# Kernel optimization log

Hardware: AMD Instinct MI355X
Metric: run time of the kernel (lower is better)

The kernel has to match this reference:

```python
import jax, jax.numpy as jnp
import numpy as np

IN_FEA = 128
OUT_FEA = 128
ALPHA = 0.2  # LeakyReLU negative slope
NEG_INF = -1.0e12


def setup_inputs() -> dict:
    key = jax.random.key(0)
    k1, k2, k3, k4 = jax.random.split(key, 4)
    b, n = 8, 2048
    inp = jax.random.normal(k1, (b, n, IN_FEA), dtype=jnp.float32)
    adj = jax.random.randint(k2, (b, n, n), 0, 2, dtype=jnp.int32)
    # xavier_uniform with gain=1.414
    def xavier(k, shape, gain=1.414):
        fan_in, fan_out = shape[0], shape[1]
        limit = gain * np.sqrt(6.0 / (fan_in + fan_out))
        return jax.random.uniform(k, shape, jnp.float32, -limit, limit)
    W = xavier(k3, (IN_FEA, OUT_FEA))
    a = xavier(k4, (2 * OUT_FEA, 1))
    return {"inp": inp, "adj": adj, "W": W, "a": a}


def reference(inp, adj, W, a):
    # h: [b, n, d]
    h = jnp.matmul(inp, W)
    # Original builds [b, n*n, 2d] via repeat/view; equivalently split a into
    # a1 (applied to h_j, the 'chunks' half) and a2 (applied to h_i).
    d = h.shape[-1]
    a1 = a[:d, 0]   # [d]
    a2 = a[d:, 0]   # [d]
    f1 = jnp.einsum('bnd,d->bn', h, a1)  # contributes per-column (j)
    f2 = jnp.einsum('bnd,d->bn', h, a2)  # contributes per-row (i)
    e = jax.nn.leaky_relu(f2[:, :, None] + f1[:, None, :], negative_slope=ALPHA)  # [b, n, n]
    logits = jnp.where(adj > 0, e, NEG_INF)
    attention = jax.nn.softmax(logits, axis=-1)
    out_h = jnp.matmul(attention, h)
    out_h = jax.nn.elu(out_h) + h  # concat=True branch
    return out_h
```

## Files before the change

### kernel.cpp

```cpp
#include <hip/hip_runtime.h>
#include <hip/hip_bf16.h>

typedef __bf16 bf16x8 __attribute__((ext_vector_type(8)));
typedef __bf16 bf16x4 __attribute__((ext_vector_type(4)));
typedef float  f32x4  __attribute__((ext_vector_type(4)));

#define LRELU_ALPHA 0.2f
#define LOG2E 1.44269504088896340736f

__device__ __forceinline__ float fexp2(float x) { return exp2f(x); }

__device__ __forceinline__ void wg_barrier() {
    asm volatile("s_waitcnt lgkmcnt(0)" ::: "memory");
    __builtin_amdgcn_s_barrier();
    asm volatile("" ::: "memory");
}

__global__ __launch_bounds__(128) void gat_prep(
    const float* __restrict__ inp, const float* __restrict__ W,
    const float* __restrict__ a,
    float* __restrict__ h, float* __restrict__ f1, float* __restrict__ f2)
{
    const int r0 = blockIdx.x << 3;
    const int d  = threadIdx.x;
    __shared__ float sIn[8][128];
    __shared__ float sRed[8][4];
    #pragma unroll
    for (int r = 0; r < 8; ++r)
        sIn[r][d] = inp[(size_t)(r0 + r) * 128 + d];
    __syncthreads();

    float acc[8] = {0.f,0.f,0.f,0.f,0.f,0.f,0.f,0.f};
    #pragma unroll 4
    for (int k = 0; k < 128; ++k) {
        float wv = W[k * 128 + d];
        #pragma unroll
        for (int r = 0; r < 8; ++r) acc[r] += sIn[r][k] * wv;
    }

    const float a1 = a[d], a2 = a[128 + d];
    const int wv = d >> 6;
    #pragma unroll
    for (int r = 0; r < 8; ++r) {
        h[(size_t)(r0 + r) * 128 + d] = acc[r];
        float t1 = acc[r] * a1;
        float t2 = acc[r] * a2;
        #pragma unroll
        for (int m = 1; m < 64; m <<= 1) {
            t1 += __shfl_xor(t1, m);
            t2 += __shfl_xor(t2, m);
        }
        if ((d & 63) == 0) { sRed[r][wv] = t1; sRed[r][2 + wv] = t2; }
    }
    __syncthreads();
    if (d < 8) {
        f1[r0 + d] = (sRed[d][0] + sRed[d][1]) * LOG2E;
        f2[r0 + d] = (sRed[d][2] + sRed[d][3]) * LOG2E;
    }
}

__global__ __launch_bounds__(256) void gat_f1max(
    const float* __restrict__ f1, float* __restrict__ f1max)
{
    const int b = blockIdx.x;
    const int t = threadIdx.x;
    float m = -1e30f;
    for (int j = t; j < 2048; j += 256) m = fmaxf(m, f1[b * 2048 + j]);
    #pragma unroll
    for (int k = 1; k < 64; k <<= 1) m = fmaxf(m, __shfl_xor(m, k));
    __shared__ float sm[4];
    if ((t & 63) == 0) sm[t >> 6] = m;
    __syncthreads();
    if (t == 0) f1max[b] = fmaxf(fmaxf(sm[0], sm[1]), fmaxf(sm[2], sm[3]));
}

__global__ __launch_bounds__(256) void gat_pack(
    const float* __restrict__ h, __bf16* __restrict__ pack)
{
    __shared__ __bf16 tile[64][74];
    const int tid = threadIdx.x;
    const int bidx = blockIdx.x;
    const int b  = bidx >> 6;
    const int tI = bidx & 63;
    const int n0 = (tI >> 1) << 6;
    const int d0 = (tI & 1) << 6;
    #pragma unroll
    for (int pass = 0; pass < 2; ++pass) {
        int row = (tid >> 3) + (pass << 5);
        int c   = (tid & 7) << 3;
        const float* src = h + (size_t)(b * 2048 + n0 + row) * 128 + d0 + c;
        float4 v0 = *(const float4*)src;
        float4 v1 = *(const float4*)(src + 4);
        __bf16* tp = &tile[row][c];
        tp[0]=(__bf16)v0.x; tp[1]=(__bf16)v0.y; tp[2]=(__bf16)v0.z; tp[3]=(__bf16)v0.w;
        tp[4]=(__bf16)v1.x; tp[5]=(__bf16)v1.y; tp[6]=(__bf16)v1.z; tp[7]=(__bf16)v1.w;
    }
    __syncthreads();
    const int lane = tid & 63;
    const int il = lane & 15;
    const int kg = lane >> 4;
    #pragma unroll
    for (int pass = 0; pass < 2; ++pass) {
        const int f  = (tid >> 6) + (pass << 2);
        const int Dl = f >> 1;
        const int jh = f & 1;
        union { __bf16 e[8]; bf16x8 v; } u;
        #pragma unroll
        for (int e = 0; e < 8; ++e)
            u.e[e] = tile[(jh << 5) + (kg << 3) + e][(Dl << 4) + il];
        const size_t off = (((size_t)(b << 5) + (n0 >> 6)) << 13)
                         + ((size_t)((((d0 >> 4) + Dl) << 1) | jh) << 9)
                         + (lane << 3);
        *(bf16x8*)(pack + off) = u.v;
    }
}

#define PCOMPUTE(TT, BUF) do {                                                \
    float4 fv = *(const float4*)&f1s[((TT) << 6) + (pj4 << 2)];               \
    float p0, p1, p2, p3;                                                     \
    { float x = f2v + fv.x; float e = fmaxf(x, LRELU_ALPHA * x) - Mshift;     \
      p0 = fexp2(__builtin_fmaf(e, (float)gA.x, -1000.f)); }                  \
    { float x = f2v + fv.y; float e = fmaxf(x, LRELU_ALPHA * x) - Mshift;     \
      p1 = fexp2(__builtin_fmaf(e, (float)gA.y, -1000.f)); }                  \
    { float x = f2v + fv.z; float e = fmaxf(x, LRELU_ALPHA * x) - Mshift;     \
      p2 = fexp2(__builtin_fmaf(e, (float)gA.z, -1000.f)); }                  \
    { float x = f2v + fv.w; float e = fmaxf(x, LRELU_ALPHA * x) - Mshift;     \
      p3 = fexp2(__builtin_fmaf(e, (float)gA.w, -1000.f)); }                  \
    bf16x4 pb;                                                                \
    pb[0] = (__bf16)p0; pb[1] = (__bf16)p1;                                   \
    pb[2] = (__bf16)p2; pb[3] = (__bf16)p3;                                   \
    den += (float)pb[0] + (float)pb[1] + (float)pb[2] + (float)pb[3];         \
    *(bf16x4*)(&Ps[BUF][pwo]) = pb;                                           \
} while (0)

__global__ __launch_bounds__(512, 4) void gat_attn5(
    const int* __restrict__ adj, const float* __restrict__ h,
    const __bf16* __restrict__ pack, const float* __restrict__ f1g,
    const float* __restrict__ f2g, const float* __restrict__ f1maxg,
    float* __restrict__ out)
{
    const int bid = ((blockIdx.x & 7) << 6) | (blockIdx.x >> 3);
    const int b  = bid >> 6;
    const int i0 = (bid & 63) << 5;
    const int tid = threadIdx.x;

    __shared__ float f1s[2048];
    __shared__ alignas(16) __bf16 Ps[2][2048];
    __shared__ float lsum[32];

    *(float4*)&f1s[tid << 2] = *(const float4*)&f1g[(b << 11) + (tid << 2)];

    const int pi  = tid >> 4;
    const int pj4 = tid & 15;
    const float fm  = f1maxg[b];
    const float f2v = f2g[(b << 11) + i0 + pi];
    const float Mshift = fmaxf(f2v + fm, LRELU_ALPHA * (f2v + fm)) - 1000.0f;
    const int* ajp = adj + (((size_t)(b << 11) + i0 + pi) << 11) + (pj4 << 2);
    const int pwo = (pi << 6) + ((((pj4 << 3)) ^ ((pi & 7) << 4)) >> 1);

    const int w    = tid >> 6;
    const int lane = tid & 63;
    const int il   = lane & 15;
    const int kg   = lane >> 4;
    const int ig   = w & 1;
    const int dq   = w >> 1;
    const int ai   = (ig << 4) + il;
    const int aof0 = (ai << 6) + (((kg << 4) ^ ((ai & 7) << 4)) >> 1);
    const int aof1 = (ai << 6) + (((64 | (kg << 4)) ^ ((ai & 7) << 4)) >> 1);
    const __bf16* pB = pack + (((size_t)b << 5) << 13) + (dq << 11) + (lane << 3);

    f32x4 acc0 = {0.f,0.f,0.f,0.f}, acc1 = {0.f,0.f,0.f,0.f};
    float den = 0.f;

    int4 gA  = *(const int4*)ajp;
    int4 gA2 = *(const int4*)(ajp + 64);
    bf16x8 Bc0 = *(const bf16x8*)(pB);
    bf16x8 Bc1 = *(const bf16x8*)(pB + 512);
    bf16x8 Bc2 = *(const bf16x8*)(pB + 1024);
    bf16x8 Bc3 = *(const bf16x8*)(pB + 1536);

    wg_barrier();

    PCOMPUTE(0, 0);
    gA = gA2;
    gA2 = *(const int4*)(ajp + 128);

    wg_barrier();

    for (int t = 0; t < 31; ++t) {
        const __bf16* pBn = pB + ((size_t)(t + 1) << 13);
        bf16x8 Bn0 = *(const bf16x8*)(pBn);
        bf16x8 Bn1 = *(const bf16x8*)(pBn + 512);
        bf16x8 Bn2 = *(const bf16x8*)(pBn + 1024);
        bf16x8 Bn3 = *(const bf16x8*)(pBn + 1536);

        bf16x8 A0 = *(const bf16x8*)(&Ps[t & 1][aof0]);
        bf16x8 A1 = *(const bf16x8*)(&Ps[t & 1][aof1]);

        PCOMPUTE(t + 1, (t + 1) & 1);
        gA = gA2;
        gA2 = *(const int4*)(ajp + (((t + 3) & 31) << 6));

        acc0 = __builtin_amdgcn_mfma_f32_16x16x32_bf16(A0, Bc0, acc0, 0, 0, 0);
        acc0 = __builtin_amdgcn_mfma_f32_16x16x32_bf16(A1, Bc1, acc0, 0, 0, 0);
        acc1 = __builtin_amdgcn_mfma_f32_16x16x32_bf16(A0, Bc2, acc1, 0, 0, 0);
        acc1 = __builtin_amdgcn_mfma_f32_16x16x32_bf16(A1, Bc3, acc1, 0, 0, 0);

        Bc0 = Bn0; Bc1 = Bn1; Bc2 = Bn2; Bc3 = Bn3;

        wg_barrier();
    }

    {
        bf16x8 A0 = *(const bf16x8*)(&Ps[1][aof0]);
        bf16x8 A1 = *(const bf16x8*)(&Ps[1][aof1]);
        acc0 = __builtin_amdgcn_mfma_f32_16x16x32_bf16(A0, Bc0, acc0, 0, 0, 0);
        acc0 = __builtin_amdgcn_mfma_f32_16x16x32_bf16(A1, Bc1, acc0, 0, 0, 0);
        acc1 = __builtin_amdgcn_mfma_f32_16x16x32_bf16(A0, Bc2, acc1, 0, 0, 0);
        acc1 = __builtin_amdgcn_mfma_f32_16x16x32_bf16(A1, Bc3, acc1, 0, 0, 0);
    }

    den += __shfl_xor(den, 1);
    den += __shfl_xor(den, 2);
    den += __shfl_xor(den, 4);
    den += __shfl_xor(den, 8);
    if (pj4 == 0) lsum[pi] = den;
    wg_barrier();

    #pragma unroll
    for (int r = 0; r < 4; ++r) {
        const int   row = (kg << 2) + r;
        const float dn  = lsum[(ig << 4) + row];
        const size_t gbase = (((size_t)(b << 11) + i0 + (ig << 4) + row) << 7)
                             + (dq << 5) + il;
        float v, e;
        v = acc0[r] / dn; e = (v > 0.f) ? v : (__expf(v) - 1.f); out[gbase]      = e + h[gbase];
        v = acc1[r] / dn; e = (v > 0.f) ? v : (__expf(v) - 1.f); out[gbase + 16] = e + h[gbase + 16];
    }
}

extern "C" void kernel_launch(void* const* d_in, const int* in_sizes, int n_in,
                              void* d_out, int out_size, void* d_ws, size_t ws_size,
                              hipStream_t stream)
{
    const float* inp = (const float*)d_in[0];
    const int*   adj = (const int*)d_in[1];
    const float* W   = (const float*)d_in[2];
    const float* a   = (const float*)d_in[3];
    float* out = (float*)d_out;

    char* ws = (char*)d_ws;
    float*  h     = (float*)ws;
    __bf16* pack  = (__bf16*)(ws + 8388608);
    float*  f1    = (float*)(ws + 8388608 + 4194304);
    float*  f2    = (float*)(ws + 8388608 + 4194304 + 65536);
    float*  f1max = (float*)(ws + 8388608 + 4194304 + 131072);

    gat_prep<<<2048, 128, 0, stream>>>(inp, W, a, h, f1, f2);
    gat_f1max<<<8, 256, 0, stream>>>(f1, f1max);
    gat_pack<<<512, 256, 0, stream>>>(h, pack);
    gat_attn5<<<512, 512, 0, stream>>>(adj, h, pack, f1, f2, f1max, out);
}
```

Baseline: 59.60 us.

## Bit-pack adjacency in a pre-pass and store h as bf16

Adds a gat_adjpack kernel that streams the int32 adjacency once and writes a 1-bit-per-edge mask in the nibble layout the attention kernel consumes. The attention kernel then reads one uint4 per thread instead of prefetching int4 adjacency tiles every iteration. h is now written once as bf16, which shrinks the pack and residual reads, and each wave now covers 32 rows by 16 features so B fragments load half as often. The full adjacency read still happens, just in a separate simple kernel, and the residual add now uses bf16-rounded h, which loses some precision.

```diff
diff --git a/kernel.cpp b/kernel.cpp
--- a/kernel.cpp
+++ b/kernel.cpp
@@ -19,7 +19,7 @@
 __global__ __launch_bounds__(128) void gat_prep(
     const float* __restrict__ inp, const float* __restrict__ W,
     const float* __restrict__ a,
-    float* __restrict__ h, float* __restrict__ f1, float* __restrict__ f2)
+    __bf16* __restrict__ hb, float* __restrict__ f1, float* __restrict__ f2)
 {
     const int r0 = blockIdx.x << 3;
     const int d  = threadIdx.x;
@@ -42,7 +42,7 @@
     const int wv = d >> 6;
     #pragma unroll
     for (int r = 0; r < 8; ++r) {
-        h[(size_t)(r0 + r) * 128 + d] = acc[r];
+        hb[(size_t)(r0 + r) * 128 + d] = (__bf16)acc[r];
         float t1 = acc[r] * a1;
         float t2 = acc[r] * a2;
         #pragma unroll
@@ -75,9 +75,9 @@
 }
 
 __global__ __launch_bounds__(256) void gat_pack(
-    const float* __restrict__ h, __bf16* __restrict__ pack)
-{
-    __shared__ __bf16 tile[64][74];
+    const __bf16* __restrict__ hb, __bf16* __restrict__ pack)
+{
+    __shared__ __bf16 tile[64][72];
     const int tid = threadIdx.x;
     const int bidx = blockIdx.x;
     const int b  = bidx >> 6;
@@ -88,12 +88,8 @@
     for (int pass = 0; pass < 2; ++pass) {
         int row = (tid >> 3) + (pass << 5);
         int c   = (tid & 7) << 3;
-        const float* src = h + (size_t)(b * 2048 + n0 + row) * 128 + d0 + c;
-        float4 v0 = *(const float4*)src;
-        float4 v1 = *(const float4*)(src + 4);
-        __bf16* tp = &tile[row][c];
-        tp[0]=(__bf16)v0.x; tp[1]=(__bf16)v0.y; tp[2]=(__bf16)v0.z; tp[3]=(__bf16)v0.w;
-        tp[4]=(__bf16)v1.x; tp[5]=(__bf16)v1.y; tp[6]=(__bf16)v1.z; tp[7]=(__bf16)v1.w;
+        *(bf16x8*)&tile[row][c] =
+            *(const bf16x8*)(hb + (size_t)(b * 2048 + n0 + row) * 128 + d0 + c);
     }
     __syncthreads();
     const int lane = tid & 63;
@@ -115,17 +111,78 @@
     }
 }
 
+__global__ __launch_bounds__(256) void gat_adjpack(
+    const int* __restrict__ adj, unsigned int* __restrict__ tb)
+{
+    __shared__ unsigned long long blt[16][8][4];
+    const int tid  = threadIdx.x;
+    const int w    = tid >> 6;
+    const int lane = tid & 63;
+    const int base = blockIdx.x << 4;
+
+    #pragma unroll
+    for (int rr = 0; rr < 4; ++rr) {
+        const int rloc = (w << 2) + rr;
+        const int* ap = adj + ((size_t)(base + rloc) << 11) + (lane << 2);
+        unsigned long long kept = 0ull;
+        #pragma unroll
+        for (int s = 0; s < 8; ++s) {
+            int4 v = *(const int4*)(ap + (s << 8));
+            unsigned long long b0 = __ballot(v.x > 0);
+            unsigned long long b1 = __ballot(v.y > 0);
+            unsigned long long b2 = __ballot(v.z > 0);
+            unsigned long long b3 = __ballot(v.w > 0);
+            const int e4 = lane & 3;
+            unsigned long long be = (e4 == 0) ? b0 : (e4 == 1) ? b1
+                                  : (e4 == 2) ? b2 : b3;
+            kept = ((lane >> 2) == s) ? be : kept;
+        }
+        if (lane < 32) blt[rloc][lane >> 2][lane & 3] = kept;
+    }
+    __syncthreads();
+
+    const int r   = tid >> 4;
+    const int pj4 = tid & 15;
+    unsigned int w0 = 0, w1 = 0, w2 = 0, w3 = 0;
+    #pragma unroll
+    for (int s = 0; s < 8; ++s) {
+        unsigned long long q0 = blt[r][s][0];
+        unsigned long long q1 = blt[r][s][1];
+        unsigned long long q2 = blt[r][s][2];
+        unsigned long long q3 = blt[r][s][3];
+        #pragma unroll
+        for (int tt = 0; tt < 4; ++tt) {
+            const int t = (s << 2) + tt;
+            const int L = (tt << 4) + pj4;
+            unsigned int nib = (unsigned int)((q0 >> L) & 1)
+                             | ((unsigned int)((q1 >> L) & 1) << 1)
+                             | ((unsigned int)((q2 >> L) & 1) << 2)
+                             | ((unsigned int)((q3 >> L) & 1) << 3);
+            const unsigned int sh = (unsigned int)((t & 7) << 2);
+            if (t < 8)       w0 |= nib << sh;
+            else if (t < 16) w1 |= nib << sh;
+            else if (t < 24) w2 |= nib << sh;
+            else             w3 |= nib << sh;
+        }
+    }
+    uint4 o; o.x = w0; o.y = w1; o.z = w2; o.w = w3;
+    *(uint4*)(tb + (((size_t)(base + r) << 4) + pj4) * 4) = o;
+}
+
 #define PCOMPUTE(TT, BUF) do {                                                \
     float4 fv = *(const float4*)&f1s[((TT) << 6) + (pj4 << 2)];               \
+    const unsigned int wv = ((TT) & 16) ? (((TT) & 8) ? aw.w : aw.z)          \
+                                        : (((TT) & 8) ? aw.y : aw.x);         \
+    const unsigned int nib = wv >> (((TT) & 7) << 2);                         \
     float p0, p1, p2, p3;                                                     \
-    { float x = f2v + fv.x; float e = fmaxf(x, LRELU_ALPHA * x) - Mshift;     \
-      p0 = fexp2(__builtin_fmaf(e, (float)gA.x, -1000.f)); }                  \
-    { float x = f2v + fv.y; float e = fmaxf(x, LRELU_ALPHA * x) - Mshift;     \
-      p1 = fexp2(__builtin_fmaf(e, (float)gA.y, -1000.f)); }                  \
-    { float x = f2v + fv.z; float e = fmaxf(x, LRELU_ALPHA * x) - Mshift;     \
-      p2 = fexp2(__builtin_fmaf(e, (float)gA.z, -1000.f)); }                  \
-    { float x = f2v + fv.w; float e = fmaxf(x, LRELU_ALPHA * x) - Mshift;     \
-      p3 = fexp2(__builtin_fmaf(e, (float)gA.w, -1000.f)); }                  \
+    { float x = f2v + fv.x; float e1 = fmaxf(x, LRELU_ALPHA * x) - Mshift;    \
+      p0 = fexp2(__builtin_fmaf(e1, (float)(nib & 1), -1000.f)); }            \
+    { float x = f2v + fv.y; float e1 = fmaxf(x, LRELU_ALPHA * x) - Mshift;    \
+      p1 = fexp2(__builtin_fmaf(e1, (float)((nib >> 1) & 1), -1000.f)); }     \
+    { float x = f2v + fv.z; float e1 = fmaxf(x, LRELU_ALPHA * x) - Mshift;    \
+      p2 = fexp2(__builtin_fmaf(e1, (float)((nib >> 2) & 1), -1000.f)); }     \
+    { float x = f2v + fv.w; float e1 = fmaxf(x, LRELU_ALPHA * x) - Mshift;    \
+      p3 = fexp2(__builtin_fmaf(e1, (float)((nib >> 3) & 1), -1000.f)); }     \
     bf16x4 pb;                                                                \
     pb[0] = (__bf16)p0; pb[1] = (__bf16)p1;                                   \
     pb[2] = (__bf16)p2; pb[3] = (__bf16)p3;                                   \
@@ -133,8 +190,8 @@
     *(bf16x4*)(&Ps[BUF][pwo]) = pb;                                           \
 } while (0)
 
-__global__ __launch_bounds__(512, 4) void gat_attn5(
-    const int* __restrict__ adj, const float* __restrict__ h,
+__global__ __launch_bounds__(512, 4) void gat_attn6(
+    const unsigned int* __restrict__ tb, const __bf16* __restrict__ hb,
     const __bf16* __restrict__ pack, const float* __restrict__ f1g,
     const float* __restrict__ f2g, const float* __restrict__ f1maxg,
     float* __restrict__ out)
@@ -155,35 +212,27 @@
     const float fm  = f1maxg[b];
     const float f2v = f2g[(b << 11) + i0 + pi];
     const float Mshift = fmaxf(f2v + fm, LRELU_ALPHA * (f2v + fm)) - 1000.0f;
-    const int* ajp = adj + (((size_t)(b << 11) + i0 + pi) << 11) + (pj4 << 2);
     const int pwo = (pi << 6) + ((((pj4 << 3)) ^ ((pi & 7) << 4)) >> 1);
+
+    const uint4 aw = *(const uint4*)(tb + ((((size_t)(b << 11) + i0 + pi) << 4) + pj4) * 4);
 
     const int w    = tid >> 6;
     const int lane = tid & 63;
     const int il   = lane & 15;
     const int kg   = lane >> 4;
-    const int ig   = w & 1;
-    const int dq   = w >> 1;
-    const int ai   = (ig << 4) + il;
-    const int aof0 = (ai << 6) + (((kg << 4) ^ ((ai & 7) << 4)) >> 1);
-    const int aof1 = (ai << 6) + (((64 | (kg << 4)) ^ ((ai & 7) << 4)) >> 1);
-    const __bf16* pB = pack + (((size_t)b << 5) << 13) + (dq << 11) + (lane << 3);
+    const int aof0 = (il << 6) + (((kg << 4) ^ ((il & 7) << 4)) >> 1);
+    const int aof1 = (il << 6) + (((64 | (kg << 4)) ^ ((il & 7) << 4)) >> 1);
+    const __bf16* pB = pack + ((size_t)b << 18) + (w << 10) + (lane << 3);
 
     f32x4 acc0 = {0.f,0.f,0.f,0.f}, acc1 = {0.f,0.f,0.f,0.f};
     float den = 0.f;
 
-    int4 gA  = *(const int4*)ajp;
-    int4 gA2 = *(const int4*)(ajp + 64);
     bf16x8 Bc0 = *(const bf16x8*)(pB);
     bf16x8 Bc1 = *(const bf16x8*)(pB + 512);
-    bf16x8 Bc2 = *(const bf16x8*)(pB + 1024);
-    bf16x8 Bc3 = *(const bf16x8*)(pB + 1536);
 
     wg_barrier();
 
     PCOMPUTE(0, 0);
-    gA = gA2;
-    gA2 = *(const int4*)(ajp + 128);
 
     wg_barrier();
 
@@ -191,33 +240,33 @@
         const __bf16* pBn = pB + ((size_t)(t + 1) << 13);
         bf16x8 Bn0 = *(const bf16x8*)(pBn);
         bf16x8 Bn1 = *(const bf16x8*)(pBn + 512);
-        bf16x8 Bn2 = *(const bf16x8*)(pBn + 1024);
-        bf16x8 Bn3 = *(const bf16x8*)(pBn + 1536);
-
-        bf16x8 A0 = *(const bf16x8*)(&Ps[t & 1][aof0]);
-        bf16x8 A1 = *(const bf16x8*)(&Ps[t & 1][aof1]);
+
+        bf16x8 A00 = *(const bf16x8*)(&Ps[t & 1][aof0]);
+        bf16x8 A01 = *(const bf16x8*)(&Ps[t & 1][aof1]);
+        bf16x8 A10 = *(const bf16x8*)(&Ps[t & 1][aof0 + 1024]);
+        bf16x8 A11 = *(const bf16x8*)(&Ps[t & 1][aof1 + 1024]);
 
         PCOMPUTE(t + 1, (t + 1) & 1);
-        gA = gA2;
-        gA2 = *(const int4*)(ajp + (((t + 3) & 31) << 6));
-
-        acc0 = __builtin_amdgcn_mfma_f32_16x16x32_bf16(A0, Bc0, acc0, 0, 0, 0);
-        acc0 = __builtin_amdgcn_mfma_f32_16x16x32_bf16(A1, Bc1, acc0, 0, 0, 0);
-        acc1 = __builtin_amdgcn_mfma_f32_16x16x32_bf16(A0, Bc2, acc1, 0, 0, 0);
-        acc1 = __builtin_amdgcn_mfma_f32_16x16x32_bf16(A1, Bc3, acc1, 0, 0, 0);
-
-        Bc0 = Bn0; Bc1 = Bn1; Bc2 = Bn2; Bc3 = Bn3;
+
+        acc0 = __builtin_amdgcn_mfma_f32_16x16x32_bf16(A00, Bc0, acc0, 0, 0, 0);
+        acc0 = __builtin_amdgcn_mfma_f32_16x16x32_bf16(A01, Bc1, acc0, 0, 0, 0);
+        acc1 = __builtin_amdgcn_mfma_f32_16x16x32_bf16(A10, Bc0, acc1, 0, 0, 0);
+        acc1 = __builtin_amdgcn_mfma_f32_16x16x32_bf16(A11, Bc1, acc1, 0, 0, 0);
+
+        Bc0 = Bn0; Bc1 = Bn1;
 
         wg_barrier();
     }
 
     {
-        bf16x8 A0 = *(const bf16x8*)(&Ps[1][aof0]);
-        bf16x8 A1 = *(const bf16x8*)(&Ps[1][aof1]);
-        acc0 = __builtin_amdgcn_mfma_f32_16x16x32_bf16(A0, Bc0, acc0, 0, 0, 0);
-        acc0 = __builtin_amdgcn_mfma_f32_16x16x32_bf16(A1, Bc1, acc0, 0, 0, 0);
-        acc1 = __builtin_amdgcn_mfma_f32_16x16x32_bf16(A0, Bc2, acc1, 0, 0, 0);
-        acc1 = __builtin_amdgcn_mfma_f32_16x16x32_bf16(A1, Bc3, acc1, 0, 0, 0);
+        bf16x8 A00 = *(const bf16x8*)(&Ps[1][aof0]);
+        bf16x8 A01 = *(const bf16x8*)(&Ps[1][aof1]);
+        bf16x8 A10 = *(const bf16x8*)(&Ps[1][aof0 + 1024]);
+        bf16x8 A11 = *(const bf16x8*)(&Ps[1][aof1 + 1024]);
+        acc0 = __builtin_amdgcn_mfma_f32_16x16x32_bf16(A00, Bc0, acc0, 0, 0, 0);
+        acc0 = __builtin_amdgcn_mfma_f32_16x16x32_bf16(A01, Bc1, acc0, 0, 0, 0);
+        acc1 = __builtin_amdgcn_mfma_f32_16x16x32_bf16(A10, Bc0, acc1, 0, 0, 0);
+        acc1 = __builtin_amdgcn_mfma_f32_16x16x32_bf16(A11, Bc1, acc1, 0, 0, 0);
     }
 
     den += __shfl_xor(den, 1);
@@ -229,13 +278,17 @@
 
     #pragma unroll
     for (int r = 0; r < 4; ++r) {
-        const int   row = (kg << 2) + r;
-        const float dn  = lsum[(ig << 4) + row];
-        const size_t gbase = (((size_t)(b << 11) + i0 + (ig << 4) + row) << 7)
-                             + (dq << 5) + il;
+        const int row0 = (kg << 2) + r;
+        const int row1 = row0 + 16;
+        const float dn0 = lsum[row0];
+        const float dn1 = lsum[row1];
+        const size_t g0 = (((size_t)(b << 11) + i0 + row0) << 7) + (w << 4) + il;
+        const size_t g1 = (((size_t)(b << 11) + i0 + row1) << 7) + (w << 4) + il;
         float v, e;
-        v = acc0[r] / dn; e = (v > 0.f) ? v : (__expf(v) - 1.f); out[gbase]      = e + h[gbase];
-        v = acc1[r] / dn; e = (v > 0.f) ? v : (__expf(v) - 1.f); out[gbase + 16] = e + h[gbase + 16];
+        v = acc0[r] / dn0; e = (v > 0.f) ? v : (__expf(v) - 1.f);
+        out[g0] = e + (float)hb[g0];
+        v = acc1[r] / dn1; e = (v > 0.f) ? v : (__expf(v) - 1.f);
+        out[g1] = e + (float)hb[g1];
     }
 }
 
@@ -250,14 +303,16 @@
     float* out = (float*)d_out;
 
     char* ws = (char*)d_ws;
-    float*  h     = (float*)ws;
-    __bf16* pack  = (__bf16*)(ws + 8388608);
-    float*  f1    = (float*)(ws + 8388608 + 4194304);
-    float*  f2    = (float*)(ws + 8388608 + 4194304 + 65536);
-    float*  f1max = (float*)(ws + 8388608 + 4194304 + 131072);
-
-    gat_prep<<<2048, 128, 0, stream>>>(inp, W, a, h, f1, f2);
+    __bf16*       hb    = (__bf16*)ws;
+    __bf16*       pack  = (__bf16*)(ws + (4 << 20));
+    unsigned int* tb    = (unsigned int*)(ws + (8 << 20));
+    float*        f1    = (float*)(ws + (12 << 20));
+    float*        f2    = (float*)(ws + (12 << 20) + 65536);
+    float*        f1max = (float*)(ws + (12 << 20) + 131072);
+
+    gat_adjpack<<<1024, 256, 0, stream>>>(adj, tb);
+    gat_prep<<<2048, 128, 0, stream>>>(inp, W, a, hb, f1, f2);
     gat_f1max<<<8, 256, 0, stream>>>(f1, f1max);
-    gat_pack<<<512, 256, 0, stream>>>(h, pack);
-    gat_attn5<<<512, 512, 0, stream>>>(adj, h, pack, f1, f2, f1max, out);
-}
+    gat_pack<<<512, 256, 0, stream>>>(hb, pack);
+    gat_attn6<<<512, 512, 0, stream>>>(tb, hb, pack, f1, f2, f1max, out);
+}
```

After: 78.43 us. 1.32x slower.

## Bit-pack adjacency up front and compute probabilities in registers feeding MFMA directly

Applied to the files above, without the earlier changes.

The attention kernel now streams the block's adjacency rows once at the start and packs them into a shared-memory bitmask. Each wave then computes its own softmax numerators straight into MFMA A-operand registers, which removes the Ps shared-memory round trip and the per-tile workgroup barriers. The row denominator comes from an extra MFMA against a ones vector instead of shuffle reductions. The intermediate h is also stored as bf16 to halve its traffic, using the raw v_exp instruction. In exchange, the exp work is duplicated across the four waves sharing the same rows, and the residual add uses bf16-precision h.

```diff
diff --git a/kernel.cpp b/kernel.cpp
--- a/kernel.cpp
+++ b/kernel.cpp
@@ -2,13 +2,18 @@
 #include <hip/hip_bf16.h>
 
 typedef __bf16 bf16x8 __attribute__((ext_vector_type(8)));
-typedef __bf16 bf16x4 __attribute__((ext_vector_type(4)));
 typedef float  f32x4  __attribute__((ext_vector_type(4)));
 
 #define LRELU_ALPHA 0.2f
 #define LOG2E 1.44269504088896340736f
 
-__device__ __forceinline__ float fexp2(float x) { return exp2f(x); }
+__device__ __forceinline__ float fexp2(float x) {
+#if __has_builtin(__builtin_amdgcn_exp2f)
+    return __builtin_amdgcn_exp2f(x);
+#else
+    float r; asm("v_exp_f32 %0, %1" : "=v"(r) : "v"(x)); return r;
+#endif
+}
 
 __device__ __forceinline__ void wg_barrier() {
     asm volatile("s_waitcnt lgkmcnt(0)" ::: "memory");
@@ -19,7 +24,7 @@
 __global__ __launch_bounds__(128) void gat_prep(
     const float* __restrict__ inp, const float* __restrict__ W,
     const float* __restrict__ a,
-    float* __restrict__ h, float* __restrict__ f1, float* __restrict__ f2)
+    __bf16* __restrict__ hb, float* __restrict__ f1, float* __restrict__ f2)
 {
     const int r0 = blockIdx.x << 3;
     const int d  = threadIdx.x;
@@ -42,7 +47,7 @@
     const int wv = d >> 6;
     #pragma unroll
     for (int r = 0; r < 8; ++r) {
-        h[(size_t)(r0 + r) * 128 + d] = acc[r];
+        hb[(size_t)(r0 + r) * 128 + d] = (__bf16)acc[r];
         float t1 = acc[r] * a1;
         float t2 = acc[r] * a2;
         #pragma unroll
@@ -75,9 +80,9 @@
 }
 
 __global__ __launch_bounds__(256) void gat_pack(
-    const float* __restrict__ h, __bf16* __restrict__ pack)
-{
-    __shared__ __bf16 tile[64][74];
+    const __bf16* __restrict__ hb, __bf16* __restrict__ pack)
+{
+    __shared__ __bf16 tile[64][72];
     const int tid = threadIdx.x;
     const int bidx = blockIdx.x;
     const int b  = bidx >> 6;
@@ -88,12 +93,8 @@
     for (int pass = 0; pass < 2; ++pass) {
         int row = (tid >> 3) + (pass << 5);
         int c   = (tid & 7) << 3;
-        const float* src = h + (size_t)(b * 2048 + n0 + row) * 128 + d0 + c;
-        float4 v0 = *(const float4*)src;
-        float4 v1 = *(const float4*)(src + 4);
-        __bf16* tp = &tile[row][c];
-        tp[0]=(__bf16)v0.x; tp[1]=(__bf16)v0.y; tp[2]=(__bf16)v0.z; tp[3]=(__bf16)v0.w;
-        tp[4]=(__bf16)v1.x; tp[5]=(__bf16)v1.y; tp[6]=(__bf16)v1.z; tp[7]=(__bf16)v1.w;
+        *(bf16x8*)&tile[row][c] =
+            *(const bf16x8*)(hb + (size_t)(b * 2048 + n0 + row) * 128 + d0 + c);
     }
     __syncthreads();
     const int lane = tid & 63;
@@ -115,26 +116,15 @@
     }
 }
 
-#define PCOMPUTE(TT, BUF) do {                                                \
-    float4 fv = *(const float4*)&f1s[((TT) << 6) + (pj4 << 2)];               \
-    float p0, p1, p2, p3;                                                     \
-    { float x = f2v + fv.x; float e = fmaxf(x, LRELU_ALPHA * x) - Mshift;     \
-      p0 = fexp2(__builtin_fmaf(e, (float)gA.x, -1000.f)); }                  \
-    { float x = f2v + fv.y; float e = fmaxf(x, LRELU_ALPHA * x) - Mshift;     \
-      p1 = fexp2(__builtin_fmaf(e, (float)gA.y, -1000.f)); }                  \
-    { float x = f2v + fv.z; float e = fmaxf(x, LRELU_ALPHA * x) - Mshift;     \
-      p2 = fexp2(__builtin_fmaf(e, (float)gA.z, -1000.f)); }                  \
-    { float x = f2v + fv.w; float e = fmaxf(x, LRELU_ALPHA * x) - Mshift;     \
-      p3 = fexp2(__builtin_fmaf(e, (float)gA.w, -1000.f)); }                  \
-    bf16x4 pb;                                                                \
-    pb[0] = (__bf16)p0; pb[1] = (__bf16)p1;                                   \
-    pb[2] = (__bf16)p2; pb[3] = (__bf16)p3;                                   \
-    den += (float)pb[0] + (float)pb[1] + (float)pb[2] + (float)pb[3];         \
-    *(bf16x4*)(&Ps[BUF][pwo]) = pb;                                           \
-} while (0)
-
-__global__ __launch_bounds__(512, 4) void gat_attn5(
-    const int* __restrict__ adj, const float* __restrict__ h,
+__device__ __forceinline__ float pone(float fv, unsigned int by, int e,
+                                      float C1p, float C2p) {
+    float arg = fmaxf(fv + C1p, __builtin_fmaf(LRELU_ALPHA, fv, C2p));
+    float mk  = (float)((by >> e) & 1u);
+    return fexp2(__builtin_fmaf(arg, mk, -1000.f));
+}
+
+__global__ __launch_bounds__(512, 4) void gat_attn8(
+    const int* __restrict__ adj, const __bf16* __restrict__ hb,
     const __bf16* __restrict__ pack, const float* __restrict__ f1g,
     const float* __restrict__ f2g, const float* __restrict__ f1maxg,
     float* __restrict__ out)
@@ -145,18 +135,25 @@
     const int tid = threadIdx.x;
 
     __shared__ float f1s[2048];
-    __shared__ alignas(16) __bf16 Ps[2][2048];
-    __shared__ float lsum[32];
+    __shared__ unsigned int bits[32 * 68];
 
     *(float4*)&f1s[tid << 2] = *(const float4*)&f1g[(b << 11) + (tid << 2)];
 
-    const int pi  = tid >> 4;
-    const int pj4 = tid & 15;
-    const float fm  = f1maxg[b];
-    const float f2v = f2g[(b << 11) + i0 + pi];
-    const float Mshift = fmaxf(f2v + fm, LRELU_ALPHA * (f2v + fm)) - 1000.0f;
-    const int* ajp = adj + (((size_t)(b << 11) + i0 + pi) << 11) + (pj4 << 2);
-    const int pwo = (pi << 6) + ((((pj4 << 3)) ^ ((pi & 7) << 4)) >> 1);
+    {
+        const int* abase = adj + (((size_t)((b << 11) + i0)) << 11) + (tid << 2);
+        int4 c0 = *(const int4*)(abase);
+        int4 c1 = *(const int4*)(abase + 2048);
+        for (int p = 0; p < 32; ++p) {
+            int4 c2 = *(const int4*)(abase + (((p + 2) & 31) << 11));
+            unsigned int u = (unsigned)(c0.x > 0)        | ((unsigned)(c0.y > 0) << 1)
+                           | ((unsigned)(c0.z > 0) << 2) | ((unsigned)(c0.w > 0) << 3);
+            u |= ((unsigned)__shfl_xor((int)u, 1)) << 4;
+            u |= ((unsigned)__shfl_xor((int)u, 2)) << 8;
+            u |= ((unsigned)__shfl_xor((int)u, 4)) << 16;
+            if ((tid & 7) == 0) bits[p * 68 + (tid >> 3)] = u;
+            c0 = c1; c1 = c2;
+        }
+    }
 
     const int w    = tid >> 6;
     const int lane = tid & 63;
@@ -164,16 +161,28 @@
     const int kg   = lane >> 4;
     const int ig   = w & 1;
     const int dq   = w >> 1;
-    const int ai   = (ig << 4) + il;
-    const int aof0 = (ai << 6) + (((kg << 4) ^ ((ai & 7) << 4)) >> 1);
-    const int aof1 = (ai << 6) + (((64 | (kg << 4)) ^ ((ai & 7) << 4)) >> 1);
-    const __bf16* pB = pack + (((size_t)b << 5) << 13) + (dq << 11) + (lane << 3);
+    const int row  = (ig << 4) + il;
+
+    const float fm  = f1maxg[b];
+    const float f2v = f2g[(b << 11) + i0 + row];
+    const float z   = f2v + fm;
+    const float M   = fmaxf(z, LRELU_ALPHA * z);
+    const float C1p = f2v - M + 1000.f;
+    const float C2p = __builtin_fmaf(LRELU_ALPHA, f2v, 1000.f - M);
+
+    const unsigned char* bitsB = (const unsigned char*)bits;
+    const int rb  = row * 272 + kg;
+    const int kgo = kg << 3;
+
+    const __bf16* pB = pack + ((size_t)b << 18) + (dq << 11) + (lane << 3);
 
     f32x4 acc0 = {0.f,0.f,0.f,0.f}, acc1 = {0.f,0.f,0.f,0.f};
-    float den = 0.f;
-
-    int4 gA  = *(const int4*)ajp;
-    int4 gA2 = *(const int4*)(ajp + 64);
+    f32x4 accd = {0.f,0.f,0.f,0.f};
+    union { __bf16 e[8]; bf16x8 v; } ones;
+    #pragma unroll
+    for (int x = 0; x < 8; ++x) ones.e[x] = (__bf16)1.0f;
+    const bf16x8 onesv = ones.v;
+
     bf16x8 Bc0 = *(const bf16x8*)(pB);
     bf16x8 Bc1 = *(const bf16x8*)(pB + 512);
     bf16x8 Bc2 = *(const bf16x8*)(pB + 1024);
@@ -181,61 +190,59 @@
 
     wg_barrier();
 
-    PCOMPUTE(0, 0);
-    gA = gA2;
-    gA2 = *(const int4*)(ajp + 128);
-
-    wg_barrier();
-
-    for (int t = 0; t < 31; ++t) {
-        const __bf16* pBn = pB + ((size_t)(t + 1) << 13);
+    for (int t = 0; t < 32; ++t) {
+        const __bf16* pBn = pB + ((size_t)((t + 1) & 31) << 13);
         bf16x8 Bn0 = *(const bf16x8*)(pBn);
         bf16x8 Bn1 = *(const bf16x8*)(pBn + 512);
         bf16x8 Bn2 = *(const bf16x8*)(pBn + 1024);
         bf16x8 Bn3 = *(const bf16x8*)(pBn + 1536);
 
-        bf16x8 A0 = *(const bf16x8*)(&Ps[t & 1][aof0]);
-        bf16x8 A1 = *(const bf16x8*)(&Ps[t & 1][aof1]);
-
-        PCOMPUTE(t + 1, (t + 1) & 1);
-        gA = gA2;
-        gA2 = *(const int4*)(ajp + (((t + 3) & 31) << 6));
-
-        acc0 = __builtin_amdgcn_mfma_f32_16x16x32_bf16(A0, Bc0, acc0, 0, 0, 0);
-        acc0 = __builtin_amdgcn_mfma_f32_16x16x32_bf16(A1, Bc1, acc0, 0, 0, 0);
-        acc1 = __builtin_amdgcn_mfma_f32_16x16x32_bf16(A0, Bc2, acc1, 0, 0, 0);
-        acc1 = __builtin_amdgcn_mfma_f32_16x16x32_bf16(A1, Bc3, acc1, 0, 0, 0);
+        const unsigned int by0 = bitsB[rb + (t << 3)];
+        const unsigned int by1 = bitsB[rb + (t << 3) + 4];
+        float4 fa = *(const float4*)&f1s[(t << 6) + kgo];
+        float4 fb = *(const float4*)&f1s[(t << 6) + kgo + 4];
+        float4 fc = *(const float4*)&f1s[(t << 6) + 32 + kgo];
+        float4 fd = *(const float4*)&f1s[(t << 6) + 32 + kgo + 4];
+
+        union { __bf16 e[8]; bf16x8 v; } pa0, pa1;
+        pa0.e[0] = (__bf16)pone(fa.x, by0, 0, C1p, C2p);
+        pa0.e[1] = (__bf16)pone(fa.y, by0, 1, C1p, C2p);
+        pa0.e[2] = (__bf16)pone(fa.z, by0, 2, C1p, C2p);
+        pa0.e[3] = (__bf16)pone(fa.w, by0, 3, C1p, C2p);
+        pa0.e[4] = (__bf16)pone(fb.x, by0, 4, C1p, C2p);
+        pa0.e[5] = (__bf16)pone(fb.y, by0, 5, C1p, C2p);
+        pa0.e[6] = (__bf16)pone(fb.z, by0, 6, C1p, C2p);
+        pa0.e[7] = (__bf16)pone(fb.w, by0, 7, C1p, C2p);
+        pa1.e[0] = (__bf16)pone(fc.x, by1, 0, C1p, C2p);
+        pa1.e[1] = (__bf16)pone(fc.y, by1, 1, C1p, C2p);
+        pa1.e[2] = (__bf16)pone(fc.z, by1, 2, C1p, C2p);
+        pa1.e[3] = (__bf16)pone(fc.w, by1, 3, C1p, C2p);
+        pa1.e[4] = (__bf16)pone(fd.x, by1, 4, C1p, C2p);
+        pa1.e[5] = (__bf16)pone(fd.y, by1, 5, C1p, C2p);
+        pa1.e[6] = (__bf16)pone(fd.z, by1, 6, C1p, C2p);
+        pa1.e[7] = (__bf16)pone(fd.w, by1, 7, C1p, C2p);
+
+        acc0 = __builtin_amdgcn_mfma_f32_16x16x32_bf16(pa0.v, Bc0, acc0, 0, 0, 0);
+        acc0 = __builtin_amdgcn_mfma_f32_16x16x32_bf16(pa1.v, Bc1, acc0, 0, 0, 0);
+        acc1 = __builtin_amdgcn_mfma_f32_16x16x32_bf16(pa0.v, Bc2, acc1, 0, 0, 0);
+        acc1 = __builtin_amdgcn_mfma_f32_16x16x32_bf16(pa1.v, Bc3, acc1, 0, 0, 0);
+        accd = __builtin_amdgcn_mfma_f32_16x16x32_bf16(pa0.v, onesv, accd, 0, 0, 0);
+        accd = __builtin_amdgcn_mfma_f32_16x16x32_bf16(pa1.v, onesv, accd, 0, 0, 0);
 
         Bc0 = Bn0; Bc1 = Bn1; Bc2 = Bn2; Bc3 = Bn3;
-
-        wg_barrier();
-    }
-
-    {
-        bf16x8 A0 = *(const bf16x8*)(&Ps[1][aof0]);
-        bf16x8 A1 = *(const bf16x8*)(&Ps[1][aof1]);
-        acc0 = __builtin_amdgcn_mfma_f32_16x16x32_bf16(A0, Bc0, acc0, 0, 0, 0);
-        acc0 = __builtin_amdgcn_mfma_f32_16x16x32_bf16(A1, Bc1, acc0, 0, 0, 0);
-        acc1 = __builtin_amdgcn_mfma_f32_16x16x32_bf16(A0, Bc2, acc1, 0, 0, 0);
-        acc1 = __builtin_amdgcn_mfma_f32_16x16x32_bf16(A1, Bc3, acc1, 0, 0, 0);
-    }
-
-    den += __shfl_xor(den, 1);
-    den += __shfl_xor(den, 2);
-    den += __shfl_xor(den, 4);
-    den += __shfl_xor(den, 8);
-    if (pj4 == 0) lsum[pi] = den;
-    wg_barrier();
+    }
 
     #pragma unroll
     for (int r = 0; r < 4; ++r) {
-        const int   row = (kg << 2) + r;
-        const float dn  = lsum[(ig << 4) + row];
-        const size_t gbase = (((size_t)(b << 11) + i0 + (ig << 4) + row) << 7)
-                             + (dq << 5) + il;
+        const int orow = (kg << 2) + r;
+        const float dn = accd[r];
+        const size_t g0 = (((size_t)(b << 11) + i0 + (ig << 4) + orow) << 7)
+                          + (dq << 5) + il;
         float v, e;
-        v = acc0[r] / dn; e = (v > 0.f) ? v : (__expf(v) - 1.f); out[gbase]      = e + h[gbase];
-        v = acc1[r] / dn; e = (v > 0.f) ? v : (__expf(v) - 1.f); out[gbase + 16] = e + h[gbase + 16];
+        v = acc0[r] / dn; e = (v > 0.f) ? v : (__expf(v) - 1.f);
+        out[g0] = e + (float)hb[g0];
+        v = acc1[r] / dn; e = (v > 0.f) ? v : (__expf(v) - 1.f);
+        out[g0 + 16] = e + (float)hb[g0 + 16];
     }
 }
 
@@ -250,14 +257,14 @@
     float* out = (float*)d_out;
 
     char* ws = (char*)d_ws;
-    float*  h     = (float*)ws;
-    __bf16* pack  = (__bf16*)(ws + 8388608);
-    float*  f1    = (float*)(ws + 8388608 + 4194304);
-    float*  f2    = (float*)(ws + 8388608 + 4194304 + 65536);
-    float*  f1max = (float*)(ws + 8388608 + 4194304 + 131072);
-
-    gat_prep<<<2048, 128, 0, stream>>>(inp, W, a, h, f1, f2);
+    __bf16* hb    = (__bf16*)ws;
+    __bf16* pack  = (__bf16*)(ws + (4 << 20));
+    float*  f1    = (float*)(ws + (8 << 20));
+    float*  f2    = (float*)(ws + (8 << 20) + 65536);
+    float*  f1max = (float*)(ws + (8 << 20) + 131072);
+
+    gat_prep<<<2048, 128, 0, stream>>>(inp, W, a, hb, f1, f2);
     gat_f1max<<<8, 256, 0, stream>>>(f1, f1max);
-    gat_pack<<<512, 256, 0, stream>>>(h, pack);
-    gat_attn5<<<512, 512, 0, stream>>>(adj, h, pack, f1, f2, f1max, out);
-}
+    gat_pack<<<512, 256, 0, stream>>>(hb, pack);
+    gat_attn8<<<512, 512, 0, stream>>>(adj, hb, pack, f1, f2, f1max, out);
+}
```

Result: slower. 88.55 us (+48.6%).

## Factor softmax exponent into precomputed per-row and per-column exp2 terms

Applied to the files above, without the earlier changes.

The exponential of the LeakyReLU logit is factored into products. Each block precomputes exp2(f1) and exp2(alpha*f1) per column and exp2 scale factors per row, so the inner loop needs only a compare, a multiply and an adjacency select, with no exp per element. The intermediate h is also stored in bf16 instead of fp32, which halves the prep/pack traffic and the residual read. exp2 now uses the raw hardware instruction. The trade-off is lower precision in the residual term and a possible overflow or underflow risk in the factored exponentials.

```diff
diff --git a/kernel.cpp b/kernel.cpp
--- a/kernel.cpp
+++ b/kernel.cpp
@@ -8,7 +8,13 @@
 #define LRELU_ALPHA 0.2f
 #define LOG2E 1.44269504088896340736f
 
-__device__ __forceinline__ float fexp2(float x) { return exp2f(x); }
+__device__ __forceinline__ float fexp2(float x) {
+#if __has_builtin(__builtin_amdgcn_exp2f)
+    return __builtin_amdgcn_exp2f(x);
+#else
+    float r; asm("v_exp_f32 %0, %1" : "=v"(r) : "v"(x)); return r;
+#endif
+}
 
 __device__ __forceinline__ void wg_barrier() {
     asm volatile("s_waitcnt lgkmcnt(0)" ::: "memory");
@@ -19,7 +25,7 @@
 __global__ __launch_bounds__(128) void gat_prep(
     const float* __restrict__ inp, const float* __restrict__ W,
     const float* __restrict__ a,
-    float* __restrict__ h, float* __restrict__ f1, float* __restrict__ f2)
+    __bf16* __restrict__ hb, float* __restrict__ f1, float* __restrict__ f2)
 {
     const int r0 = blockIdx.x << 3;
     const int d  = threadIdx.x;
@@ -42,7 +48,7 @@
     const int wv = d >> 6;
     #pragma unroll
     for (int r = 0; r < 8; ++r) {
-        h[(size_t)(r0 + r) * 128 + d] = acc[r];
+        hb[(size_t)(r0 + r) * 128 + d] = (__bf16)acc[r];
         float t1 = acc[r] * a1;
         float t2 = acc[r] * a2;
         #pragma unroll
@@ -75,9 +81,9 @@
 }
 
 __global__ __launch_bounds__(256) void gat_pack(
-    const float* __restrict__ h, __bf16* __restrict__ pack)
-{
-    __shared__ __bf16 tile[64][74];
+    const __bf16* __restrict__ hb, __bf16* __restrict__ pack)
+{
+    __shared__ __bf16 tile[64][72];
     const int tid = threadIdx.x;
     const int bidx = blockIdx.x;
     const int b  = bidx >> 6;
@@ -88,12 +94,8 @@
     for (int pass = 0; pass < 2; ++pass) {
         int row = (tid >> 3) + (pass << 5);
         int c   = (tid & 7) << 3;
-        const float* src = h + (size_t)(b * 2048 + n0 + row) * 128 + d0 + c;
-        float4 v0 = *(const float4*)src;
-        float4 v1 = *(const float4*)(src + 4);
-        __bf16* tp = &tile[row][c];
-        tp[0]=(__bf16)v0.x; tp[1]=(__bf16)v0.y; tp[2]=(__bf16)v0.z; tp[3]=(__bf16)v0.w;
-        tp[4]=(__bf16)v1.x; tp[5]=(__bf16)v1.y; tp[6]=(__bf16)v1.z; tp[7]=(__bf16)v1.w;
+        *(bf16x8*)&tile[row][c] =
+            *(const bf16x8*)(hb + (size_t)(b * 2048 + n0 + row) * 128 + d0 + c);
     }
     __syncthreads();
     const int lane = tid & 63;
@@ -116,16 +118,17 @@
 }
 
 #define PCOMPUTE(TT, BUF) do {                                                \
-    float4 fv = *(const float4*)&f1s[((TT) << 6) + (pj4 << 2)];               \
-    float p0, p1, p2, p3;                                                     \
-    { float x = f2v + fv.x; float e = fmaxf(x, LRELU_ALPHA * x) - Mshift;     \
-      p0 = fexp2(__builtin_fmaf(e, (float)gA.x, -1000.f)); }                  \
-    { float x = f2v + fv.y; float e = fmaxf(x, LRELU_ALPHA * x) - Mshift;     \
-      p1 = fexp2(__builtin_fmaf(e, (float)gA.y, -1000.f)); }                  \
-    { float x = f2v + fv.z; float e = fmaxf(x, LRELU_ALPHA * x) - Mshift;     \
-      p2 = fexp2(__builtin_fmaf(e, (float)gA.z, -1000.f)); }                  \
-    { float x = f2v + fv.w; float e = fmaxf(x, LRELU_ALPHA * x) - Mshift;     \
-      p3 = fexp2(__builtin_fmaf(e, (float)gA.w, -1000.f)); }                  \
+    const int _jb = ((TT) << 6) + (pj4 << 2);                                 \
+    float4 uu = *(const float4*)&us[_jb];                                     \
+    float4 vv = *(const float4*)&vs[_jb];                                     \
+    float p0 = (uu.x > ti) ? ai * uu.x : bi * vv.x;                           \
+    float p1 = (uu.y > ti) ? ai * uu.y : bi * vv.y;                           \
+    float p2 = (uu.z > ti) ? ai * uu.z : bi * vv.z;                           \
+    float p3 = (uu.w > ti) ? ai * uu.w : bi * vv.w;                           \
+    p0 = (gA.x > 0) ? p0 : 0.f;                                               \
+    p1 = (gA.y > 0) ? p1 : 0.f;                                               \
+    p2 = (gA.z > 0) ? p2 : 0.f;                                               \
+    p3 = (gA.w > 0) ? p3 : 0.f;                                               \
     bf16x4 pb;                                                                \
     pb[0] = (__bf16)p0; pb[1] = (__bf16)p1;                                   \
     pb[2] = (__bf16)p2; pb[3] = (__bf16)p3;                                   \
@@ -133,8 +136,8 @@
     *(bf16x4*)(&Ps[BUF][pwo]) = pb;                                           \
 } while (0)
 
-__global__ __launch_bounds__(512, 4) void gat_attn5(
-    const int* __restrict__ adj, const float* __restrict__ h,
+__global__ __launch_bounds__(512, 4) void gat_attn11(
+    const int* __restrict__ adj, const __bf16* __restrict__ hb,
     const __bf16* __restrict__ pack, const float* __restrict__ f1g,
     const float* __restrict__ f2g, const float* __restrict__ f1maxg,
     float* __restrict__ out)
@@ -144,17 +147,31 @@
     const int i0 = (bid & 63) << 5;
     const int tid = threadIdx.x;
 
-    __shared__ float f1s[2048];
+    __shared__ float us[2048];
+    __shared__ float vs[2048];
     __shared__ alignas(16) __bf16 Ps[2][2048];
     __shared__ float lsum[32];
 
-    *(float4*)&f1s[tid << 2] = *(const float4*)&f1g[(b << 11) + (tid << 2)];
+    {
+        float4 fv = *(const float4*)&f1g[(b << 11) + (tid << 2)];
+        float4 uu, vv;
+        uu.x = fexp2(fv.x); uu.y = fexp2(fv.y);
+        uu.z = fexp2(fv.z); uu.w = fexp2(fv.w);
+        vv.x = fexp2(LRELU_ALPHA * fv.x); vv.y = fexp2(LRELU_ALPHA * fv.y);
+        vv.z = fexp2(LRELU_ALPHA * fv.z); vv.w = fexp2(LRELU_ALPHA * fv.w);
+        *(float4*)&us[tid << 2] = uu;
+        *(float4*)&vs[tid << 2] = vv;
+    }
 
     const int pi  = tid >> 4;
     const int pj4 = tid & 15;
     const float fm  = f1maxg[b];
     const float f2v = f2g[(b << 11) + i0 + pi];
-    const float Mshift = fmaxf(f2v + fm, LRELU_ALPHA * (f2v + fm)) - 1000.0f;
+    const float z   = f2v + fm;
+    const float M   = fmaxf(z, LRELU_ALPHA * z);
+    const float ai  = fexp2(f2v - M);
+    const float bi  = fexp2(__builtin_fmaf(LRELU_ALPHA, f2v, -M));
+    const float ti  = fexp2(-f2v);
     const int* ajp = adj + (((size_t)(b << 11) + i0 + pi) << 11) + (pj4 << 2);
     const int pwo = (pi << 6) + ((((pj4 << 3)) ^ ((pi & 7) << 4)) >> 1);
 
@@ -164,9 +181,9 @@
     const int kg   = lane >> 4;
     const int ig   = w & 1;
     const int dq   = w >> 1;
-    const int ai   = (ig << 4) + il;
-    const int aof0 = (ai << 6) + (((kg << 4) ^ ((ai & 7) << 4)) >> 1);
-    const int aof1 = (ai << 6) + (((64 | (kg << 4)) ^ ((ai & 7) << 4)) >> 1);
+    const int ai2  = (ig << 4) + il;
+    const int aof0 = (ai2 << 6) + (((kg << 4) ^ ((ai2 & 7) << 4)) >> 1);
+    const int aof1 = (ai2 << 6) + (((64 | (kg << 4)) ^ ((ai2 & 7) << 4)) >> 1);
     const __bf16* pB = pack + (((size_t)b << 5) << 13) + (dq << 11) + (lane << 3);
 
     f32x4 acc0 = {0.f,0.f,0.f,0.f}, acc1 = {0.f,0.f,0.f,0.f};
@@ -234,8 +251,10 @@
         const size_t gbase = (((size_t)(b << 11) + i0 + (ig << 4) + row) << 7)
                              + (dq << 5) + il;
         float v, e;
-        v = acc0[r] / dn; e = (v > 0.f) ? v : (__expf(v) - 1.f); out[gbase]      = e + h[gbase];
-        v = acc1[r] / dn; e = (v > 0.f) ? v : (__expf(v) - 1.f); out[gbase + 16] = e + h[gbase + 16];
+        v = acc0[r] / dn; e = (v > 0.f) ? v : (__expf(v) - 1.f);
+        out[gbase] = e + (float)hb[gbase];
+        v = acc1[r] / dn; e = (v > 0.f) ? v : (__expf(v) - 1.f);
+        out[gbase + 16] = e + (float)hb[gbase + 16];
     }
 }
 
@@ -250,14 +269,14 @@
     float* out = (float*)d_out;
 
     char* ws = (char*)d_ws;
-    float*  h     = (float*)ws;
-    __bf16* pack  = (__bf16*)(ws + 8388608);
-    float*  f1    = (float*)(ws + 8388608 + 4194304);
-    float*  f2    = (float*)(ws + 8388608 + 4194304 + 65536);
-    float*  f1max = (float*)(ws + 8388608 + 4194304 + 131072);
-
-    gat_prep<<<2048, 128, 0, stream>>>(inp, W, a, h, f1, f2);
+    __bf16* hb    = (__bf16*)ws;
+    __bf16* pack  = (__bf16*)(ws + (4 << 20));
+    float*  f1    = (float*)(ws + (8 << 20));
+    float*  f2    = (float*)(ws + (8 << 20) + 65536);
+    float*  f1max = (float*)(ws + (8 << 20) + 131072);
+
+    gat_prep<<<2048, 128, 0, stream>>>(inp, W, a, hb, f1, f2);
     gat_f1max<<<8, 256, 0, stream>>>(f1, f1max);
-    gat_pack<<<512, 256, 0, stream>>>(h, pack);
-    gat_attn5<<<512, 512, 0, stream>>>(adj, h, pack, f1, f2, f1max, out);
-}
+    gat_pack<<<512, 256, 0, stream>>>(hb, pack);
+    gat_attn11<<<512, 512, 0, stream>>>(adj, hb, pack, f1, f2, f1max, out);
+}
```

New measurement: 58.68 us. Within noise of the previous version (-1.6%).
